# Kernel tuning notes

Hardware: AMD Instinct MI355X
Metric: run time of the kernel (lower is better)

Reference implementation:

```python
import jax, jax.numpy as jnp
import numpy as np

TOL = 1e-3


def _image_grads(F):
    # replicate-pad central difference, matches GradientBatch (conv with [-0.5,0,0.5])
    Fx = jnp.pad(F, ((0, 0), (0, 0), (0, 0), (1, 1)), mode='edge')
    gx = 0.5 * (Fx[:, :, :, 2:] - Fx[:, :, :, :-2])
    Fy = jnp.pad(F, ((0, 0), (0, 0), (1, 1), (0, 0)), mode='edge')
    gy = 0.5 * (Fy[:, :, 2:, :] - Fy[:, :, :-2, :])
    return gx, gy


def _param_to_H(p):
    B = p.shape[0]
    z = jnp.zeros((B, 1, 1), p.dtype)
    return jnp.concatenate([p, z], 1).reshape(B, 3, 3) + jnp.eye(3, dtype=p.dtype)


def _bilinear_sample(A, xw, yw):
    # grid_sample(mode='bilinear', align_corners=True, padding_mode='zeros') at pixel coords (xw, yw)
    B, k, h, w = A.shape
    x0 = jnp.floor(xw)
    y0 = jnp.floor(yw)
    fx = (xw - x0).reshape(B, 1, h * w)
    fy = (yw - y0).reshape(B, 1, h * w)
    Af = A.reshape(B, k, h * w)

    def gather(xi, yi):
        valid = (xi >= 0) & (xi <= w - 1) & (yi >= 0) & (yi <= h - 1)
        xi_c = jnp.clip(xi, 0, w - 1).astype(jnp.int32)
        yi_c = jnp.clip(yi, 0, h - 1).astype(jnp.int32)
        idx = (yi_c * w + xi_c).reshape(B, 1, h * w)
        v = jnp.take_along_axis(Af, jnp.broadcast_to(idx, (B, k, h * w)), axis=2)
        return v * valid.reshape(B, 1, h * w).astype(A.dtype)

    v00 = gather(x0, y0)
    v01 = gather(x0 + 1, y0)
    v10 = gather(x0, y0 + 1)
    v11 = gather(x0 + 1, y0 + 1)
    Q = ((1 - fx) * (1 - fy) * v00 + fx * (1 - fy) * v01
         + (1 - fx) * fy * v10 + fx * fy * v11)
    return Q.reshape(B, k, h, w)


def _deeplk(img, temp, init_param, max_itr):
    B, k, h, w = temp.shape
    dt = temp.dtype
    gx, gy = _image_grads(temp)
    # centered pixel grid (meshgrid in source: x - x.max()/2)
    x = jnp.arange(w, dtype=dt) - (w - 1) / 2.0
    y = jnp.arange(h, dtype=dt) - (h - 1) / 2.0
    X, Y = jnp.meshgrid(x, y)  # (h, w); X varies along w
    Xf = jnp.tile(X.reshape(-1), k)  # [k*h*w], tiled per channel
    Yf = jnp.tile(Y.reshape(-1), k)
    gxf = gx.reshape(B, k * h * w)
    gyf = gy.reshape(B, k * h * w)
    dIdp = jnp.stack([
        Xf * gxf, Yf * gxf, gxf,
        Xf * gyf, Yf * gyf, gyf,
        -Xf * Xf * gxf - Xf * Yf * gyf,
        -Xf * Yf * gxf - Yf * Yf * gyf,
    ], axis=2)  # [B, k*h*w, 8]
    Hmat = jnp.einsum('bnp,bnq->bpq', dIdp, dIdp)  # [B,8,8]
    invH = jnp.linalg.inv(Hmat)
    invH_dIdp = jnp.einsum('bpq,bnq->bpn', invH, dIdp)  # [B,8,k*h*w]
    xy = jnp.stack([X.reshape(-1), Y.reshape(-1), jnp.ones((h * w,), dt)], 0)  # [3, h*w]
    tolf = jnp.asarray(TOL, dt)

    def step(carry, _):
        p, dp = carry
        Hm = _param_to_H(p)
        xyw = jnp.einsum('bij,jn->bin', Hm, xy)  # [B,3,h*w]
        Xw = (xyw[:, 0] / xyw[:, 2]).reshape(B, h, w) + (w - 1) / 2.0
        Yw = (xyw[:, 1] / xyw[:, 2]).reshape(B, h, w) + (h - 1) / 2.0
        Fi_warp = _bilinear_sample(img, Xw, Yw)
        xn = Xw / ((w - 1) / 2.0) - 1.0
        yn = Yw / ((h - 1) / 2.0) - 1.0
        mask = ((xn > -1 + 2.0 / w) & (xn < 1 - 2.0 / w)
                & (yn > -1 + 2.0 / h) & (yn < 1 - 2.0 / h)).astype(dt)
        r = (Fi_warp - temp * mask[:, None]).reshape(B, k * h * w, 1)
        dp_new = jnp.einsum('bpn,bnj->bpj', invH_dIdp, r)  # [B,8,1]
        dp_new = dp_new.at[:, 6:8, 0].set(0.0)  # zero projective terms
        active = (jnp.linalg.norm(dp, axis=1, keepdims=True) > tolf).astype(dt)
        dp2 = active * dp_new  # converged samples freeze (dp stays 0)
        return (p - dp2, dp2), None

    dp0 = jnp.ones((B, 8, 1), dt)
    (p, _), _ = jax.lax.scan(step, (init_param, dp0), None, length=max_itr)
    return p


def setup_inputs() -> dict:
    key = jax.random.key(0)
    k1, k2 = jax.random.split(key)
    B, k, h, w = 8, 8, 256, 256
    img = jax.random.normal(k1, (B, k, h, w), dtype=jnp.float32)
    temp = jax.random.normal(k2, (B, k, h, w), dtype=jnp.float32)
    init_param = jnp.zeros((B, 8, 1), dtype=jnp.float32)
    return {"img": img, "temp": temp, "init_param": init_param, "max_itr": 10}


def reference(img, temp, init_param, max_itr):
    p = _deeplk(img, temp, init_param, max_itr)
    return (p, _param_to_H(p))
```

## Files before the change

### kernel.cpp

```cpp
#include <hip/hip_runtime.h>
#include <hip/hip_bf16.h>

#define B_ 8
#define K_ 8
#define H_ 256
#define W_ 256
#define HW (H_*W_)

__device__ __forceinline__ unsigned short f2bf(float f) {
    __hip_bfloat16 h = __float2bfloat16(f);
    return *reinterpret_cast<unsigned short*>(&h);
}
__device__ __forceinline__ void ub8(uint4 u, float* o) {
    o[0] = __uint_as_float(u.x << 16); o[1] = __uint_as_float(u.x & 0xffff0000u);
    o[2] = __uint_as_float(u.y << 16); o[3] = __uint_as_float(u.y & 0xffff0000u);
    o[4] = __uint_as_float(u.z << 16); o[5] = __uint_as_float(u.z & 0xffff0000u);
    o[6] = __uint_as_float(u.w << 16); o[7] = __uint_as_float(u.w & 0xffff0000u);
}
__device__ __forceinline__ float half_reduce(float v) {
    v += __shfl_down(v, 16, 64);
    v += __shfl_down(v, 8, 64);
    v += __shfl_down(v, 4, 64);
    v += __shfl_down(v, 2, 64);
    v += __shfl_down(v, 1, 64);
    return v;
}

__device__ __forceinline__ void pixel_accum(
    const uint4* __restrict__ imgT, const uint4* __restrict__ TG,
    int b, int x, int y,
    float h00, float h01, float h02, float h10, float h11, float h12,
    float h20, float h21, float* aa) {
    const int px = (y << 8) | x;
    const float X = (float)x - 127.5f, Y = (float)y - 127.5f;
    const float zw = h20 * X + h21 * Y + 1.f;
    const float Xw = (h00 * X + h01 * Y + h02) / zw + 127.5f;
    const float Yw = (h10 * X + h11 * Y + h12) / zw + 127.5f;
    const float NLO = -1.f + 2.f / 256.f, NHI = 1.f - 2.f / 256.f;
    const float xn = Xw / 127.5f - 1.f, yn = Yw / 127.5f - 1.f;
    const float m = (xn > NLO && xn < NHI && yn > NLO && yn < NHI) ? 1.f : 0.f;

    const float x0f = floorf(Xw), y0f = floorf(Yw);
    const float fx = Xw - x0f, fy = Yw - y0f;
    const float x1f = x0f + 1.f, y1f = y0f + 1.f;
    const bool vx0 = (x0f >= 0.f) && (x0f <= 255.f);
    const bool vx1 = (x1f >= 0.f) && (x1f <= 255.f);
    const bool vy0 = (y0f >= 0.f) && (y0f <= 255.f);
    const bool vy1 = (y1f >= 0.f) && (y1f <= 255.f);
    const int xi0 = (int)fminf(fmaxf(x0f, 0.f), 255.f);
    const int xi1 = (int)fminf(fmaxf(x1f, 0.f), 255.f);
    const int yi0 = (int)fminf(fmaxf(y0f, 0.f), 255.f);
    const int yi1 = (int)fminf(fmaxf(y1f, 0.f), 255.f);
    const int i00 = yi0 * W_ + xi0, i01 = yi0 * W_ + xi1;
    const int i10 = yi1 * W_ + xi0, i11 = yi1 * W_ + xi1;
    const float w00 = ((vx0 && vy0) ? 1.f : 0.f) * (1.f - fx) * (1.f - fy);
    const float w01 = ((vx1 && vy0) ? 1.f : 0.f) * fx * (1.f - fy);
    const float w10 = ((vx0 && vy1) ? 1.f : 0.f) * (1.f - fx) * fy;
    const float w11 = ((vx1 && vy1) ? 1.f : 0.f) * fx * fy;

    const int base = b * HW;
    const uint4 u00 = imgT[base + i00], u01 = imgT[base + i01];
    const uint4 u10 = imgT[base + i10], u11 = imgT[base + i11];
    const uint4* tg = TG + (size_t)(base + px) * 3;
    const uint4 t0 = tg[0], g0 = tg[1], g1 = tg[2];

    float A00[8], A01[8], A10[8], A11[8], GX[8], GY[8], TV[8];
    ub8(u00, A00); ub8(u01, A01); ub8(u10, A10); ub8(u11, A11);
    ub8(t0, TV);   ub8(g0, GX);   ub8(g1, GY);

    float vx = 0.f, vy = 0.f;
    #pragma unroll
    for (int c = 0; c < 8; ++c) {
        const float Q = w00 * A00[c] + w01 * A01[c] + w10 * A10[c] + w11 * A11[c];
        const float r = Q - TV[c] * m;
        vx += GX[c] * r;
        vy += GY[c] * r;
    }
    const float t0a = X * vx, t4a = Y * vy;
    const float cc = t0a + t4a;
    aa[0] += t0a;      aa[1] += Y * vx;  aa[2] += vx;
    aa[3] += X * vy;   aa[4] += t4a;     aa[5] += vy;
    aa[6] -= X * cc;   aa[7] -= Y * cc;
}

__global__ __launch_bounds__(256) void prep_kernel(
    const float* __restrict__ img, const float* __restrict__ temp,
    uint4* __restrict__ imgT, uint4* __restrict__ TG,
    double* __restrict__ gramP) {
    __shared__ float smem[9472];
    const int b   = blockIdx.x & 7;
    const int y   = blockIdx.x >> 3;
    const int tid = threadIdx.x;
    const int ym = (y > 0) ? y - 1 : 0;
    const int yp = (y < 255) ? y + 1 : 255;

    #pragma unroll
    for (int j = 0; j < 8; ++j) {
        const int slot = tid + 256 * j;
        const int rowid = slot >> 6, col4 = slot & 63;
        const int c = rowid >> 2, sel = rowid & 3;
        const int sy = (sel == 0) ? ym : ((sel == 2) ? yp : y);
        const float* src = ((sel == 3) ? img : temp)
                         + ((size_t)(b * K_ + c) * HW + sy * W_ + col4 * 4);
        const float4 v = *(const float4*)src;
        *(float4*)&smem[(c * 4 + sel) * 256 + col4 * 4] = v;
    }
    __syncthreads();

    const int x = tid;
    const int px = (y << 8) | x;
    const float X = (float)x - 127.5f, Y = (float)y - 127.5f;
    const int xm = (x > 0) ? x - 1 : 0;
    const int xp = (x < 255) ? x + 1 : 255;
    float Sxx = 0.f, Sxy = 0.f, Syy = 0.f;
    unsigned int imgp[4] = {0, 0, 0, 0};
    unsigned int tgp[12];
    #pragma unroll
    for (int i = 0; i < 12; ++i) tgp[i] = 0u;
    #pragma unroll
    for (int c = 0; c < 8; ++c) {
        const float* R = &smem[c * 1024];
        const float gx = 0.5f * (R[256 + xp] - R[256 + xm]);
        const float gy = 0.5f * (R[512 + x] - R[x]);
        const float tc = R[256 + x];
        const float iv = R[768 + x];
        Sxx += gx * gx; Sxy += gx * gy; Syy += gy * gy;
        const int sh = (c & 1) * 16;
        imgp[c >> 1]     |= ((unsigned int)f2bf(iv)) << sh;
        tgp[c >> 1]      |= ((unsigned int)f2bf(tc)) << sh;
        tgp[4 + (c >> 1)]|= ((unsigned int)f2bf(gx)) << sh;
        tgp[8 + (c >> 1)]|= ((unsigned int)f2bf(gy)) << sh;
    }
    const size_t gpx = (size_t)b * HW + px;
    imgT[gpx] = make_uint4(imgp[0], imgp[1], imgp[2], imgp[3]);
    uint4* tg = TG + gpx * 3;
    tg[0] = make_uint4(tgp[0], tgp[1], tgp[2],  tgp[3]);
    tg[1] = make_uint4(tgp[4], tgp[5], tgp[6],  tgp[7]);
    tg[2] = make_uint4(tgp[8], tgp[9], tgp[10], tgp[11]);
    __syncthreads();

    {
        const float av[8] = {X, Y, 1.f, 0.f, 0.f, 0.f, -X * X, -X * Y};
        const float bv[8] = {0.f, 0.f, 0.f, X, Y, 1.f, -X * Y, -Y * Y};
        int idx = 0;
        #pragma unroll
        for (int pi = 0; pi < 8; ++pi)
            #pragma unroll
            for (int qi = pi; qi < 8; ++qi) {
                smem[tid * 37 + idx] = av[pi] * av[qi] * Sxx
                    + (av[pi] * bv[qi] + av[qi] * bv[pi]) * Sxy
                    + bv[pi] * bv[qi] * Syy;
                ++idx;
            }
    }
    __syncthreads();
    #pragma unroll
    for (int st = 128; st >= 1; st >>= 1) {
        if (tid < st) {
            #pragma unroll
            for (int e = 0; e < 36; ++e)
                smem[tid * 37 + e] += smem[(tid + st) * 37 + e];
        }
        __syncthreads();
    }
    if (tid < 36) gramP[((size_t)b * 36 + tid) * 256 + y] = (double)smem[tid];
}

__global__ void invert_kernel(const double* __restrict__ gramP,
                              double* __restrict__ invH) {
    const int b = blockIdx.x;
    const int t = threadIdx.x;
    __shared__ double G[36];
    __shared__ double A[64];
    __shared__ double Bi[64];
    if (t < 36) {
        double acc = 0.0;
        const double* gp = gramP + ((size_t)b * 36 + t) * 256;
        for (int r = 0; r < 256; ++r) acc += gp[r];
        G[t] = acc;
    }
    __syncthreads();
    const int i = t >> 3, j = t & 7;
    const int pp = min(i, j), qq = max(i, j);
    const int tri = 8 * pp - (pp * (pp - 1)) / 2 + (qq - pp);
    A[t]  = G[tri];
    Bi[t] = (i == j) ? 1.0 : 0.0;
    __syncthreads();
    for (int k = 0; k < 8; ++k) {
        const double piv = A[k * 8 + k];
        __syncthreads();
        if (i == k) { A[t] /= piv; Bi[t] /= piv; }
        __syncthreads();
        const double f  = A[i * 8 + k];
        const double ak = A[k * 8 + j];
        const double bk = Bi[k * 8 + j];
        __syncthreads();
        if (i != k) { A[t] -= f * ak; Bi[t] -= f * bk; }
        __syncthreads();
    }
    invH[b * 64 + t] = Bi[t];
}

__global__ __launch_bounds__(256) void iter_kernel(
    const uint4* __restrict__ imgT, const uint4* __restrict__ TG,
    const double* __restrict__ invH, const float* __restrict__ init_param,
    const double* __restrict__ stateR, double* __restrict__ stateW,
    const float* __restrict__ sPrev, float* __restrict__ sNext,
    const int* __restrict__ max_itr, int iter) {
    if (iter >= *max_itr) return;
    __shared__ float red[2048];
    __shared__ float s8[8];
    __shared__ double sh_invH[64];
    __shared__ double sh_st[16];
    __shared__ double sh_pd[16];
    const int b   = blockIdx.x & 7;
    const int yb  = blockIdx.x >> 3;
    const int tid = threadIdx.x;

    if (tid < 64) sh_invH[tid] = invH[b * 64 + tid];
    if (iter > 0) {
        if (tid >= 64 && tid < 72) sh_st[tid - 64]     = stateR[b * 8 + (tid - 64)];
        if (tid >= 72 && tid < 80) sh_st[tid - 64]     = stateR[64 + b * 8 + (tid - 72)];
    }

    if (iter == 0) {
        if (tid < 8) {
            sh_pd[tid]     = (double)init_param[b * 8 + tid];
            sh_pd[8 + tid] = 1.0;
        }
        __syncthreads();
    } else {
        const float* sR = sPrev + b * 512;
        const int e = tid >> 5, l = tid & 31;
        float v = sR[e * 64 + l] + sR[e * 64 + 32 + l];
        v = half_reduce(v);
        if ((tid & 31) == 0) s8[tid >> 5] = v;
        __syncthreads();
        if (tid < 8) {
            double nrm2 = 0.0;
            #pragma unroll
            for (int k2 = 0; k2 < 8; ++k2) {
                const double d = sh_st[8 + k2];
                nrm2 += d * d;
            }
            double dpn = 0.0;
            if (tid < 6) {
                #pragma unroll
                for (int k2 = 0; k2 < 8; ++k2)
                    dpn += sh_invH[tid * 8 + k2] * (double)s8[k2];
            }
            const double dp2 = (sqrt(nrm2) > 1e-3) ? dpn : 0.0;
            sh_pd[tid]     = sh_st[tid] - dp2;
            sh_pd[8 + tid] = dp2;
        }
        __syncthreads();
    }
    if (yb == 0 && tid < 8) {
        stateW[b * 8 + tid]      = sh_pd[tid];
        stateW[64 + b * 8 + tid] = sh_pd[8 + tid];
    }

    const float h00 = 1.f + (float)sh_pd[0], h01 = (float)sh_pd[1], h02 = (float)sh_pd[2];
    const float h10 = (float)sh_pd[3], h11 = 1.f + (float)sh_pd[4], h12 = (float)sh_pd[5];
    const float h20 = (float)sh_pd[6], h21 = (float)sh_pd[7];

    float aa[8];
    #pragma unroll
    for (int e = 0; e < 8; ++e) aa[e] = 0.f;
    #pragma unroll 1
    for (int sub = 0; sub < 4; ++sub) {
        pixel_accum(imgT, TG, b, tid, yb * 4 + sub,
                    h00, h01, h02, h10, h11, h12, h20, h21, aa);
    }

    #pragma unroll
    for (int e = 0; e < 8; ++e) red[e * 256 + tid] = aa[e];
    __syncthreads();
    {
        const int e = tid >> 5, l = tid & 31;
        float v = 0.f;
        #pragma unroll
        for (int j = 0; j < 8; ++j) v += red[e * 256 + l + 32 * j];
        v = half_reduce(v);
        if ((tid & 31) == 0) sNext[b * 512 + e * 64 + yb] = v;
    }
}

__global__ void output_kernel(const double* __restrict__ invH,
                              const float* __restrict__ init_param,
                              const double* __restrict__ st0,
                              const double* __restrict__ st1,
                              const float* __restrict__ sP0,
                              const float* __restrict__ sP1,
                              const int* __restrict__ max_itr,
                              float* __restrict__ out) {
    const int b   = blockIdx.x;
    const int tid = threadIdx.x;
    const int mi_raw = *max_itr;
    const int mi = (mi_raw > 10) ? 10 : mi_raw;
    if (mi <= 0) {
        if (tid < 8) out[b * 8 + tid] = init_param[b * 8 + tid];
        if (tid < 9) {
            float v = (tid < 8) ? init_param[b * 8 + tid] : 0.f;
            if (tid == 0 || tid == 4 || tid == 8) v += 1.f;
            out[64 + b * 9 + tid] = v;
        }
        return;
    }
    const int pr = (mi - 1) & 1;
    const double* st = pr ? st1 : st0;
    const float*  sP = pr ? sP1 : sP0;
    __shared__ float s8[8];
    __shared__ float sh_pf[8];
    const float* sb = sP + b * 512;
    const int e = tid >> 5, l = tid & 31;
    float v = sb[e * 64 + l] + sb[e * 64 + 32 + l];
    v = half_reduce(v);
    if ((tid & 31) == 0) s8[tid >> 5] = v;
    __syncthreads();
    if (tid < 8) {
        double nrm2 = 0.0;
        #pragma unroll
        for (int k2 = 0; k2 < 8; ++k2) {
            const double d = st[64 + b * 8 + k2];
            nrm2 += d * d;
        }
        double dpn = 0.0;
        if (tid < 6) {
            #pragma unroll
            for (int k2 = 0; k2 < 8; ++k2)
                dpn += invH[b * 64 + tid * 8 + k2] * (double)s8[k2];
        }
        const double dp2 = (sqrt(nrm2) > 1e-3) ? dpn : 0.0;
        const float pf = (float)(st[b * 8 + tid] - dp2);
        sh_pf[tid] = pf;
        out[b * 8 + tid] = pf;
    }
    __syncthreads();
    if (tid < 9) {
        float v2 = (tid < 8) ? sh_pf[tid] : 0.f;
        if (tid == 0 || tid == 4 || tid == 8) v2 += 1.f;
        out[64 + b * 9 + tid] = v2;
    }
}

extern "C" void kernel_launch(void* const* d_in, const int* in_sizes, int n_in,
                              void* d_out, int out_size, void* d_ws, size_t ws_size,
                              hipStream_t stream) {
    const float* img        = (const float*)d_in[0];
    const float* temp       = (const float*)d_in[1];
    const float* init_param = (const float*)d_in[2];
    const int*   max_itr    = (const int*)d_in[3];
    float* out = (float*)d_out;

    char* w = (char*)d_ws;
    double* gramP = (double*)w;
    double* st0   = gramP + 73728;
    double* st1   = st0 + 128;
    double* invH  = st1 + 128;
    float*  sP0   = (float*)(invH + 512);
    float*  sP1   = sP0 + 4096;
    uint4* imgT   = (uint4*)(w + 1048576);
    uint4* TG     = (uint4*)(w + 1048576 + 8388608);

    prep_kernel<<<B_ * H_, 256, 0, stream>>>(img, temp, imgT, TG, gramP);
    invert_kernel<<<B_, 64, 0, stream>>>(gramP, invH);
    for (int it = 0; it < 10; ++it) {
        const double* stR = (it & 1) ? st0 : st1;
        double*       stW = (it & 1) ? st1 : st0;
        const float*  sR  = (it & 1) ? sP0 : sP1;
        float*        sW  = (it & 1) ? sP1 : sP0;
        iter_kernel<<<512, 256, 0, stream>>>(imgT, TG, invH, init_param,
                                             stR, stW, sR, sW, max_itr, it);
    }
    output_kernel<<<B_, 256, 0, stream>>>(invH, init_param, st0, st1,
                                          sP0, sP1, max_itr, out);
}
```

Before: 179.6 us.

## Factor per-row Gram into 15 X-power moments and fold inversion into first iteration

Measured after the change: 162.8 us, median of 2. -9.4%, faster.

```diff
diff --git a/kernel.cpp b/kernel.cpp
--- a/kernel.cpp
+++ b/kernel.cpp
@@ -87,7 +87,8 @@
     const float* __restrict__ img, const float* __restrict__ temp,
     uint4* __restrict__ imgT, uint4* __restrict__ TG,
     double* __restrict__ gramP) {
-    __shared__ float smem[9472];
+    __shared__ float smem[8192];
+    __shared__ float s15[15];
     const int b   = blockIdx.x & 7;
     const int y   = blockIdx.x >> 3;
     const int tid = threadIdx.x;
@@ -140,69 +141,63 @@
     __syncthreads();
 
     {
-        const float av[8] = {X, Y, 1.f, 0.f, 0.f, 0.f, -X * X, -X * Y};
-        const float bv[8] = {0.f, 0.f, 0.f, X, Y, 1.f, -X * Y, -Y * Y};
-        int idx = 0;
+        const float X2 = X * X;
+        const float Xp[5] = {1.f, X, X2, X2 * X, X2 * X2};
         #pragma unroll
-        for (int pi = 0; pi < 8; ++pi)
-            #pragma unroll
-            for (int qi = pi; qi < 8; ++qi) {
-                smem[tid * 37 + idx] = av[pi] * av[qi] * Sxx
-                    + (av[pi] * bv[qi] + av[qi] * bv[pi]) * Sxy
-                    + bv[pi] * bv[qi] * Syy;
-                ++idx;
-            }
-    }
-    __syncthreads();
-    #pragma unroll
-    for (int st = 128; st >= 1; st >>= 1) {
-        if (tid < st) {
-            #pragma unroll
-            for (int e = 0; e < 36; ++e)
-                smem[tid * 37 + e] += smem[(tid + st) * 37 + e];
-        }
-        __syncthreads();
-    }
-    if (tid < 36) gramP[((size_t)b * 36 + tid) * 256 + y] = (double)smem[tid];
-}
-
-__global__ void invert_kernel(const double* __restrict__ gramP,
-                              double* __restrict__ invH) {
-    const int b = blockIdx.x;
-    const int t = threadIdx.x;
-    __shared__ double G[36];
-    __shared__ double A[64];
-    __shared__ double Bi[64];
-    if (t < 36) {
-        double acc = 0.0;
-        const double* gp = gramP + ((size_t)b * 36 + t) * 256;
-        for (int r = 0; r < 256; ++r) acc += gp[r];
-        G[t] = acc;
-    }
-    __syncthreads();
-    const int i = t >> 3, j = t & 7;
-    const int pp = min(i, j), qq = max(i, j);
-    const int tri = 8 * pp - (pp * (pp - 1)) / 2 + (qq - pp);
-    A[t]  = G[tri];
-    Bi[t] = (i == j) ? 1.0 : 0.0;
-    __syncthreads();
-    for (int k = 0; k < 8; ++k) {
-        const double piv = A[k * 8 + k];
-        __syncthreads();
-        if (i == k) { A[t] /= piv; Bi[t] /= piv; }
-        __syncthreads();
-        const double f  = A[i * 8 + k];
-        const double ak = A[k * 8 + j];
-        const double bk = Bi[k * 8 + j];
-        __syncthreads();
-        if (i != k) { A[t] -= f * ak; Bi[t] -= f * bk; }
-        __syncthreads();
-    }
-    invH[b * 64 + t] = Bi[t];
+        for (int n = 0; n < 5; ++n) {
+            smem[n * 256 + tid]        = Sxx * Xp[n];
+            smem[(5 + n) * 256 + tid]  = Sxy * Xp[n];
+            smem[(10 + n) * 256 + tid] = Syy * Xp[n];
+        }
+    }
+    __syncthreads();
+    {
+        const int e = tid >> 5, l = tid & 31;
+        float v = 0.f;
+        #pragma unroll
+        for (int j = 0; j < 8; ++j) v += smem[e * 256 + l + 32 * j];
+        v = half_reduce(v);
+        if ((tid & 31) == 0) s15[e] = v;
+    }
+    if (tid < 224) {
+        const int e = 8 + (tid >> 5), l = tid & 31;
+        float v = 0.f;
+        #pragma unroll
+        for (int j = 0; j < 8; ++j) v += smem[e * 256 + l + 32 * j];
+        v = half_reduce(v);
+        if ((tid & 31) == 0) s15[e] = v;
+    }
+    __syncthreads();
+
+    if (tid < 36) {
+        const int aC[8]  = {1, 1, 1, 0, 0, 0, -1, -1};
+        const int aNX[8] = {1, 0, 0, 0, 0, 0,  2,  1};
+        const int aNY[8] = {0, 1, 0, 0, 0, 0,  0,  1};
+        const int bC[8]  = {0, 0, 0, 1, 1, 1, -1, -1};
+        const int bNX[8] = {0, 0, 0, 1, 0, 0,  1,  0};
+        const int bNY[8] = {0, 0, 0, 0, 1, 0,  1,  2};
+        const double Yd = (double)Y;
+        const double Yp2 = Yd * Yd;
+        const double Ypw[5] = {1.0, Yd, Yp2, Yp2 * Yd, Yp2 * Yp2};
+        int p = 0, rem = tid;
+        while (rem >= 8 - p) { rem -= 8 - p; ++p; }
+        const int q = p + rem;
+        double g = 0.0;
+        const int ac = aC[p] * aC[q];
+        if (ac) g += ac * Ypw[aNY[p] + aNY[q]] * (double)s15[aNX[p] + aNX[q]];
+        const int ab1 = aC[p] * bC[q];
+        if (ab1) g += ab1 * Ypw[aNY[p] + bNY[q]] * (double)s15[5 + aNX[p] + bNX[q]];
+        const int ab2 = bC[p] * aC[q];
+        if (ab2) g += ab2 * Ypw[bNY[p] + aNY[q]] * (double)s15[5 + bNX[p] + aNX[q]];
+        const int bc = bC[p] * bC[q];
+        if (bc) g += bc * Ypw[bNY[p] + bNY[q]] * (double)s15[10 + bNX[p] + bNX[q]];
+        gramP[((size_t)b * 36 + tid) * 256 + y] = g;
+    }
 }
 
 __global__ __launch_bounds__(256) void iter_kernel(
     const uint4* __restrict__ imgT, const uint4* __restrict__ TG,
+    const double* __restrict__ gramP, double* __restrict__ invHg,
     const double* __restrict__ invH, const float* __restrict__ init_param,
     const double* __restrict__ stateR, double* __restrict__ stateW,
     const float* __restrict__ sPrev, float* __restrict__ sNext,
@@ -213,14 +208,53 @@
     __shared__ double sh_invH[64];
     __shared__ double sh_st[16];
     __shared__ double sh_pd[16];
+    const int tid = threadIdx.x;
+
+    if (iter == 0 && blockIdx.x >= 512) {
+        const int b = blockIdx.x - 512;
+        __shared__ double gpart[144];
+        __shared__ double shA[64];
+        __shared__ double shB[64];
+        if (tid < 144) {
+            const int e = tid >> 2, q = tid & 3;
+            const double* gp = gramP + ((size_t)b * 36 + e) * 256 + q * 64;
+            double acc = 0.0;
+            #pragma unroll 8
+            for (int i = 0; i < 64; ++i) acc += gp[i];
+            gpart[tid] = acc;
+        }
+        __syncthreads();
+        const int i = tid >> 3, j = tid & 7;
+        if (tid < 64) {
+            const int pp = min(i, j), qq = max(i, j);
+            const int tri = 8 * pp - (pp * (pp - 1)) / 2 + (qq - pp);
+            shA[tid] = gpart[tri * 4] + gpart[tri * 4 + 1]
+                     + gpart[tri * 4 + 2] + gpart[tri * 4 + 3];
+            shB[tid] = (i == j) ? 1.0 : 0.0;
+        }
+        __syncthreads();
+        for (int k = 0; k < 8; ++k) {
+            const double piv = shA[k * 8 + k];
+            __syncthreads();
+            if (tid < 64 && i == k) { shA[tid] /= piv; shB[tid] /= piv; }
+            __syncthreads();
+            double f = 0, ak = 0, bk = 0;
+            if (tid < 64) { f = shA[i * 8 + k]; ak = shA[k * 8 + j]; bk = shB[k * 8 + j]; }
+            __syncthreads();
+            if (tid < 64 && i != k) { shA[tid] -= f * ak; shB[tid] -= f * bk; }
+            __syncthreads();
+        }
+        if (tid < 64) invHg[b * 64 + tid] = shB[tid];
+        return;
+    }
+
     const int b   = blockIdx.x & 7;
     const int yb  = blockIdx.x >> 3;
-    const int tid = threadIdx.x;
-
-    if (tid < 64) sh_invH[tid] = invH[b * 64 + tid];
+
     if (iter > 0) {
-        if (tid >= 64 && tid < 72) sh_st[tid - 64]     = stateR[b * 8 + (tid - 64)];
-        if (tid >= 72 && tid < 80) sh_st[tid - 64]     = stateR[64 + b * 8 + (tid - 72)];
+        if (tid < 64) sh_invH[tid] = invH[b * 64 + tid];
+        if (tid >= 64 && tid < 72) sh_st[tid - 64] = stateR[b * 8 + (tid - 64)];
+        if (tid >= 72 && tid < 80) sh_st[tid - 64] = stateR[64 + b * 8 + (tid - 72)];
     }
 
     if (iter == 0) {
@@ -364,14 +398,15 @@
     uint4* TG     = (uint4*)(w + 1048576 + 8388608);
 
     prep_kernel<<<B_ * H_, 256, 0, stream>>>(img, temp, imgT, TG, gramP);
-    invert_kernel<<<B_, 64, 0, stream>>>(gramP, invH);
     for (int it = 0; it < 10; ++it) {
         const double* stR = (it & 1) ? st0 : st1;
         double*       stW = (it & 1) ? st1 : st0;
         const float*  sR  = (it & 1) ? sP0 : sP1;
         float*        sW  = (it & 1) ? sP1 : sP0;
-        iter_kernel<<<512, 256, 0, stream>>>(imgT, TG, invH, init_param,
-                                             stR, stW, sR, sW, max_itr, it);
+        const int grid = (it == 0) ? 520 : 512;
+        iter_kernel<<<grid, 256, 0, stream>>>(imgT, TG, gramP, invH, invH,
+                                              init_param, stR, stW, sR, sW,
+                                              max_itr, it);
     }
     output_kernel<<<B_, 256, 0, stream>>>(invH, init_param, st0, st1,
                                           sP0, sP1, max_itr, out);
```
